# Kernel optimization log

Measured on AMD Instinct MI355X. Metric: run time of the kernel, lower is better.

Reference implementation:

```python
import jax, jax.numpy as jnp
import numpy as np
from jax import lax

INPUT, HIDDEN, OUT = 5, 32, 2

def setup_inputs() -> dict:
    key = jax.random.key(0)
    ks = jax.random.split(key, 7)
    s_ih = 1.0 / np.sqrt(HIDDEN)
    return {
        "x": jax.random.normal(ks[0], (16384, 200, INPUT), dtype=jnp.float32),
        "W_ih": jax.random.uniform(ks[1], (4 * HIDDEN, INPUT), jnp.float32, -s_ih, s_ih),
        "W_hh": jax.random.uniform(ks[2], (4 * HIDDEN, HIDDEN), jnp.float32, -s_ih, s_ih),
        "b_ih": jax.random.uniform(ks[3], (4 * HIDDEN,), jnp.float32, -s_ih, s_ih),
        "b_hh": jax.random.uniform(ks[4], (4 * HIDDEN,), jnp.float32, -s_ih, s_ih),
        "W_fc": jax.random.uniform(ks[5], (OUT, HIDDEN), jnp.float32, -s_ih, s_ih),
        "b_fc": jax.random.uniform(ks[6], (OUT,), jnp.float32, -s_ih, s_ih),
    }

def reference(x, W_ih, W_hh, b_ih, b_hh, W_fc, b_fc):
    B = x.shape[0]
    # Precompute input projections for all timesteps in one GEMM: [B,T,4H]
    x_proj = jnp.einsum("bti,gi->btg", x, W_ih) + (b_ih + b_hh)
    xs = jnp.swapaxes(x_proj, 0, 1)  # [T, B, 4H]

    def step(carry, xg):
        h, c = carry
        gates = xg + h @ W_hh.T  # [B, 4H]
        i, f, g, o = jnp.split(gates, 4, axis=-1)  # torch gate order i,f,g,o
        i = jax.nn.sigmoid(i)
        f = jax.nn.sigmoid(f)
        g = jnp.tanh(g)
        o = jax.nn.sigmoid(o)
        c = f * c + i * g
        h = o * jnp.tanh(c)
        return (h, c), None

    h0 = jnp.zeros((B, HIDDEN), x.dtype)
    c0 = jnp.zeros((B, HIDDEN), x.dtype)
    (h_n, _), _ = lax.scan(step, (h0, c0), xs)
    return h_n @ W_fc.T + b_fc  # [B, 2]
```

## Files before the change

kernel.cpp:

```cpp
#include <hip/hip_runtime.h>


typedef __bf16 bf16x8 __attribute__((ext_vector_type(8)));
typedef float  f32x4  __attribute__((ext_vector_type(4)));
typedef unsigned int u32;

constexpr int kT = 200, kIN = 5, kH = 32;
constexpr int CT   = 40;
constexpr int HSTR = 36;

union FragU {
    bf16x8 v;
    unsigned short s[8];
    u32 u[4];
};

__device__ __forceinline__ u32 bf16_rne(float f) {
    u32 u = __float_as_uint(f);
    return (u + 0x7FFFu + ((u >> 16) & 1u)) >> 16;
}
__device__ __forceinline__ float bf16f(u32 bits) { return __uint_as_float(bits << 16); }
__device__ __forceinline__ void split2(float x, u32& hi, u32& lo) {
    hi = bf16_rne(x);
    lo = bf16_rne(x - bf16f(hi));
}

__device__ __forceinline__ float sigm(float z) {
    return __builtin_amdgcn_rcpf(1.0f + __builtin_amdgcn_exp2f(-1.4426950408889634f * z));
}
__device__ __forceinline__ float tanhv(float z) {
    return fmaf(2.0f,
        __builtin_amdgcn_rcpf(1.0f + __builtin_amdgcn_exp2f(-2.8853900817779268f * z)),
        -1.0f);
}

__global__ __launch_bounds__(64, 1) void lstm_mfma(
    const float* __restrict__ x,
    const float* __restrict__ W_ih,
    const float* __restrict__ W_hh,
    const float* __restrict__ b_ih,
    const float* __restrict__ b_hh,
    const float* __restrict__ W_fc,
    const float* __restrict__ b_fc,
    float* __restrict__ out)
{
    __shared__ uint4 xbuf[CT][33];
    __shared__ u32   hbuf[16 * HSTR];

    const int lane = threadIdx.x;
    const int n16  = lane & 15;
    const int q    = lane >> 4;
    const int b0   = blockIdx.x * 16;

    bf16x8 whhh[8], whhl[8], wihf[8];
#pragma unroll
    for (int t = 0; t < 8; ++t) {
        const int r = t * 16 + n16;
        FragU H, L;
#pragma unroll
        for (int j = 0; j < 8; ++j) {
            u32 hi, lo;
            split2(W_hh[r * kH + q * 8 + j], hi, lo);
            H.s[j] = (unsigned short)hi;
            L.s[j] = (unsigned short)lo;
        }
        whhh[t] = H.v;
        whhl[t] = L.v;

        FragU F;
        F.u[0] = F.u[1] = F.u[2] = F.u[3] = 0u;
        float wr[5];
#pragma unroll
        for (int i = 0; i < 5; ++i) wr[i] = W_ih[r * kIN + i];
        u32 bh, bl;
        split2(b_ih[r] + b_hh[r], bh, bl);
        if (q == 0) {
#pragma unroll
            for (int i = 0; i < 5; ++i) F.s[i] = (unsigned short)bf16_rne(wr[i]);
#pragma unroll
            for (int i = 5; i < 8; ++i) F.s[i] = (unsigned short)bf16_rne(wr[i - 5]);
        } else if (q == 1) {
            F.s[0] = (unsigned short)bf16_rne(wr[3]);
            F.s[1] = (unsigned short)bf16_rne(wr[4]);
#pragma unroll
            for (int i = 0; i < 5; ++i) {
                u32 hi, lo; split2(wr[i], hi, lo);
                F.s[2 + i] = (unsigned short)lo;
            }
            F.s[7] = (unsigned short)bh;
        } else if (q == 2) {
            F.s[0] = (unsigned short)bl;
        }
        wihf[t] = F.v;
    }

#pragma unroll
    for (int i = 0; i < 9; ++i) hbuf[lane * 9 + i] = 0u;
    __syncthreads();

    float cst[2][4] = {{0.f, 0.f, 0.f, 0.f}, {0.f, 0.f, 0.f, 0.f}};
    const uint4* hb4 = (const uint4*)hbuf;

    for (int phase = 0; phase < kT / CT; ++phase) {
        {
            const int mm = lane >> 2, pp = lane & 3;
            const float* xrow = x + (size_t)(b0 + mm) * (kT * kIN)
                                  + (size_t)(phase * CT + pp * (CT / 4)) * kIN;
            float xv[(CT / 4) * kIN];
            const float2* xr2 = (const float2*)xrow;
#pragma unroll
            for (int i = 0; i < (CT / 4) * kIN / 2; ++i) {
                float2 v = xr2[i];
                xv[2 * i] = v.x; xv[2 * i + 1] = v.y;
            }
#pragma unroll
            for (int s5 = 0; s5 < CT / 4; ++s5) {
                u32 xh[5], xl[5];
#pragma unroll
                for (int i = 0; i < 5; ++i) split2(xv[s5 * 5 + i], xh[i], xl[i]);
                uint4 f0 = make_uint4(xh[0] | (xh[1] << 16),
                                      xh[2] | (xh[3] << 16),
                                      xh[4] | (xl[0] << 16),
                                      xl[1] | (xl[2] << 16));
                uint4 f1 = make_uint4(xl[3] | (xl[4] << 16),
                                      xh[0] | (xh[1] << 16),
                                      xh[2] | (xh[3] << 16),
                                      xh[4] | (0x3F80u << 16));
                const int tc = pp * (CT / 4) + s5;
                xbuf[tc][mm * 2 + 0] = f0;
                xbuf[tc][mm * 2 + 1] = f1;
            }
        }
        __syncthreads();

        for (int tc = 0; tc < CT; ++tc) {
            FragU xf;
            if (q < 2) {
                *(uint4*)&xf = xbuf[tc][n16 * 2 + q];
            } else if (q == 2) {
                xf.u[0] = 0x3F80u; xf.u[1] = 0u; xf.u[2] = 0u; xf.u[3] = 0u;
            } else {
                xf.u[0] = 0u; xf.u[1] = 0u; xf.u[2] = 0u; xf.u[3] = 0u;
            }

            uint4 w0 = hb4[n16 * 9 + q * 2];
            uint4 w1 = hb4[n16 * 9 + q * 2 + 1];
            FragU AH, AL;
            AH.u[0] = __builtin_amdgcn_perm(w0.y, w0.x, 0x07060302u);
            AH.u[1] = __builtin_amdgcn_perm(w0.w, w0.z, 0x07060302u);
            AH.u[2] = __builtin_amdgcn_perm(w1.y, w1.x, 0x07060302u);
            AH.u[3] = __builtin_amdgcn_perm(w1.w, w1.z, 0x07060302u);
            AL.u[0] = __builtin_amdgcn_perm(w0.y, w0.x, 0x05040100u);
            AL.u[1] = __builtin_amdgcn_perm(w0.w, w0.z, 0x05040100u);
            AL.u[2] = __builtin_amdgcn_perm(w1.y, w1.x, 0x05040100u);
            AL.u[3] = __builtin_amdgcn_perm(w1.w, w1.z, 0x05040100u);

            f32x4 acc[8];
#pragma unroll
            for (int t = 0; t < 8; ++t) {
                f32x4 a = {0.f, 0.f, 0.f, 0.f};
                a = __builtin_amdgcn_mfma_f32_16x16x32_bf16(xf.v,  wihf[t], a, 0, 0, 0);
                a = __builtin_amdgcn_mfma_f32_16x16x32_bf16(AH.v, whhh[t], a, 0, 0, 0);
                a = __builtin_amdgcn_mfma_f32_16x16x32_bf16(AH.v, whhl[t], a, 0, 0, 0);
                a = __builtin_amdgcn_mfma_f32_16x16x32_bf16(AL.v, whhh[t], a, 0, 0, 0);
                acc[t] = a;
            }

#pragma unroll
            for (int jg = 0; jg < 2; ++jg) {
#pragma unroll
                for (int r = 0; r < 4; ++r) {
                    float iv = sigm (acc[0 + jg][r]);
                    float fv = sigm (acc[2 + jg][r]);
                    float gv = tanhv(acc[4 + jg][r]);
                    float ov = sigm (acc[6 + jg][r]);
                    float cn = fmaf(fv, cst[jg][r], iv * gv);
                    cst[jg][r] = cn;
                    float hn = ov * tanhv(cn);
                    u32 hh, hl;
                    split2(hn, hh, hl);
                    hbuf[(q * 4 + r) * HSTR + n16 + 16 * jg] = (hh << 16) | hl;
                }
            }
            __syncthreads();
        }
    }

    if (lane < 32) {
        const int m = lane >> 1, o = lane & 1;
        float s = b_fc[o];
#pragma unroll
        for (int j = 0; j < kH; ++j) {
            u32 pk = hbuf[m * HSTR + j];
            float hv = bf16f(pk >> 16) + bf16f(pk & 0xFFFFu);
            s = fmaf(hv, W_fc[o * kH + j], s);
        }
        out[(size_t)(b0 + m) * 2 + o] = s;
    }
}

extern "C" void kernel_launch(void* const* d_in, const int* in_sizes, int n_in,
                              void* d_out, int out_size, void* d_ws, size_t ws_size,
                              hipStream_t stream) {
    const float* x    = (const float*)d_in[0];
    const float* W_ih = (const float*)d_in[1];
    const float* W_hh = (const float*)d_in[2];
    const float* b_ih = (const float*)d_in[3];
    const float* b_hh = (const float*)d_in[4];
    const float* W_fc = (const float*)d_in[5];
    const float* b_fc = (const float*)d_in[6];
    float* out = (float*)d_out;

    hipLaunchKernelGGL(lstm_mfma, dim3(1024), dim3(64), 0, stream,
                       x, W_ih, W_hh, b_ih, b_hh, W_fc, b_fc, out);
}
```

Before: 287.3 us.

## Split LSTM gate tiles across two waves with double-buffered split-bf16 hidden state

```diff
diff --git a/kernel.cpp b/kernel.cpp
--- a/kernel.cpp
+++ b/kernel.cpp
@@ -7,24 +7,17 @@
 
 constexpr int kT = 200, kIN = 5, kH = 32;
 constexpr int CT   = 40;
-constexpr int HSTR = 36;
-
-union FragU {
-    bf16x8 v;
-    unsigned short s[8];
-    u32 u[4];
-};
-
-__device__ __forceinline__ u32 bf16_rne(float f) {
-    u32 u = __float_as_uint(f);
-    return (u + 0x7FFFu + ((u >> 16) & 1u)) >> 16;
-}
-__device__ __forceinline__ float bf16f(u32 bits) { return __uint_as_float(bits << 16); }
-__device__ __forceinline__ void split2(float x, u32& hi, u32& lo) {
-    hi = bf16_rne(x);
-    lo = bf16_rne(x - bf16f(hi));
-}
-
+constexpr int HSTR = 40;
+
+union FragU { bf16x8 v; __bf16 b[8]; unsigned short s[8]; u32 u[4]; uint4 q4; };
+
+__device__ __forceinline__ unsigned short bfbits(__bf16 b) {
+    union { __bf16 b; unsigned short s; } u; u.b = b; return u.s;
+}
+__device__ __forceinline__ void split2(float x, __bf16& hi, __bf16& lo) {
+    hi = (__bf16)x;
+    lo = (__bf16)(x - (float)hi);
+}
 __device__ __forceinline__ float sigm(float z) {
     return __builtin_amdgcn_rcpf(1.0f + __builtin_amdgcn_exp2f(-1.4426950408889634f * z));
 }
@@ -34,7 +27,7 @@
         -1.0f);
 }
 
-__global__ __launch_bounds__(64, 1) void lstm_mfma(
+__global__ __launch_bounds__(128) void lstm_mfma2(
     const float* __restrict__ x,
     const float* __restrict__ W_ih,
     const float* __restrict__ W_hh,
@@ -45,79 +38,124 @@
     float* __restrict__ out)
 {
     __shared__ uint4 xbuf[CT][33];
-    __shared__ u32   hbuf[16 * HSTR];
-
-    const int lane = threadIdx.x;
+    __shared__ __align__(16) __bf16 hbh[2][16 * HSTR];
+    __shared__ __align__(16) __bf16 hbl[2][16 * HSTR];
+
+    const int tid  = threadIdx.x;
+    const int wv   = tid >> 6;
+    const int lane = tid & 63;
     const int n16  = lane & 15;
     const int q    = lane >> 4;
     const int b0   = blockIdx.x * 16;
 
-    bf16x8 whhh[8], whhl[8], wihf[8];
-#pragma unroll
-    for (int t = 0; t < 8; ++t) {
+    bf16x8 whhh[4], whhl[4], wihf[4];
+#pragma unroll
+    for (int g = 0; g < 4; ++g) {
+        const int t = 2 * g + wv;
         const int r = t * 16 + n16;
         FragU H, L;
 #pragma unroll
-        for (int j = 0; j < 8; ++j) {
-            u32 hi, lo;
-            split2(W_hh[r * kH + q * 8 + j], hi, lo);
-            H.s[j] = (unsigned short)hi;
-            L.s[j] = (unsigned short)lo;
-        }
-        whhh[t] = H.v;
-        whhl[t] = L.v;
+        for (int j = 0; j < 8; ++j)
+            split2(W_hh[r * kH + q * 8 + j], H.b[j], L.b[j]);
+        whhh[g] = H.v; whhl[g] = L.v;
+
+        float wr[5];
+#pragma unroll
+        for (int i = 0; i < 5; ++i) wr[i] = W_ih[r * kIN + i];
+        __bf16 bh, bl;
+        split2(b_ih[r] + b_hh[r], bh, bl);
 
         FragU F;
         F.u[0] = F.u[1] = F.u[2] = F.u[3] = 0u;
-        float wr[5];
-#pragma unroll
-        for (int i = 0; i < 5; ++i) wr[i] = W_ih[r * kIN + i];
-        u32 bh, bl;
-        split2(b_ih[r] + b_hh[r], bh, bl);
         if (q == 0) {
 #pragma unroll
-            for (int i = 0; i < 5; ++i) F.s[i] = (unsigned short)bf16_rne(wr[i]);
-#pragma unroll
-            for (int i = 5; i < 8; ++i) F.s[i] = (unsigned short)bf16_rne(wr[i - 5]);
+            for (int i = 0; i < 5; ++i) F.b[i] = (__bf16)wr[i];
+#pragma unroll
+            for (int i = 0; i < 3; ++i) F.b[5 + i] = (__bf16)wr[i];
         } else if (q == 1) {
-            F.s[0] = (unsigned short)bf16_rne(wr[3]);
-            F.s[1] = (unsigned short)bf16_rne(wr[4]);
+            F.b[0] = (__bf16)wr[3];
+            F.b[1] = (__bf16)wr[4];
 #pragma unroll
             for (int i = 0; i < 5; ++i) {
-                u32 hi, lo; split2(wr[i], hi, lo);
-                F.s[2 + i] = (unsigned short)lo;
+                __bf16 hb, lb; split2(wr[i], hb, lb);
+                F.b[2 + i] = lb;
             }
-            F.s[7] = (unsigned short)bh;
+            F.b[7] = bh;
         } else if (q == 2) {
-            F.s[0] = (unsigned short)bl;
-        }
-        wihf[t] = F.v;
-    }
-
-#pragma unroll
-    for (int i = 0; i < 9; ++i) hbuf[lane * 9 + i] = 0u;
-    __syncthreads();
-
-    float cst[2][4] = {{0.f, 0.f, 0.f, 0.f}, {0.f, 0.f, 0.f, 0.f}};
-    const uint4* hb4 = (const uint4*)hbuf;
+            F.b[0] = bl;
+        }
+        wihf[g] = F.v;
+    }
+
+    {
+        u32* z0 = (u32*)&hbh[0][0];
+        u32* z1 = (u32*)&hbl[0][0];
+        for (int i = tid; i < (16 * HSTR) / 2; i += 128) { z0[i] = 0u; z1[i] = 0u; }
+    }
+
+    float cst[4] = {0.f, 0.f, 0.f, 0.f};
+
+    const int hro = n16 * HSTR + q * 8;
+    const int hwo = (q * 4) * HSTR + n16 + 16 * wv;
+
+    auto step = [&](int tc, const __bf16* sh, const __bf16* sl,
+                    __bf16* dh, __bf16* dl) {
+        FragU xf;
+        if (q < 2) {
+            xf.q4 = xbuf[tc][n16 * 2 + q];
+        } else if (q == 2) {
+            xf.u[0] = 0x3F80u; xf.u[1] = 0u; xf.u[2] = 0u; xf.u[3] = 0u;
+        } else {
+            xf.u[0] = 0u; xf.u[1] = 0u; xf.u[2] = 0u; xf.u[3] = 0u;
+        }
+
+        bf16x8 AH = *(const bf16x8*)(sh + hro);
+        bf16x8 AL = *(const bf16x8*)(sl + hro);
+
+        f32x4 acc[4];
+#pragma unroll
+        for (int g = 0; g < 4; ++g) {
+            f32x4 a = {0.f, 0.f, 0.f, 0.f};
+            a = __builtin_amdgcn_mfma_f32_16x16x32_bf16(xf.v, wihf[g], a, 0, 0, 0);
+            a = __builtin_amdgcn_mfma_f32_16x16x32_bf16(AH,   whhh[g], a, 0, 0, 0);
+            a = __builtin_amdgcn_mfma_f32_16x16x32_bf16(AH,   whhl[g], a, 0, 0, 0);
+            a = __builtin_amdgcn_mfma_f32_16x16x32_bf16(AL,   whhh[g], a, 0, 0, 0);
+            acc[g] = a;
+        }
+
+#pragma unroll
+        for (int r = 0; r < 4; ++r) {
+            float iv = sigm (acc[0][r]);
+            float fv = sigm (acc[1][r]);
+            float gv = tanhv(acc[2][r]);
+            float ov = sigm (acc[3][r]);
+            float cn = fmaf(fv, cst[r], iv * gv);
+            cst[r] = cn;
+            float hn = ov * tanhv(cn);
+            __bf16 hh, hl;
+            split2(hn, hh, hl);
+            dh[hwo + r * HSTR] = hh;
+            dl[hwo + r * HSTR] = hl;
+        }
+        __syncthreads();
+    };
 
     for (int phase = 0; phase < kT / CT; ++phase) {
         {
-            const int mm = lane >> 2, pp = lane & 3;
+            const int mm = tid >> 3, pp = tid & 7;
             const float* xrow = x + (size_t)(b0 + mm) * (kT * kIN)
-                                  + (size_t)(phase * CT + pp * (CT / 4)) * kIN;
-            float xv[(CT / 4) * kIN];
-            const float2* xr2 = (const float2*)xrow;
-#pragma unroll
-            for (int i = 0; i < (CT / 4) * kIN / 2; ++i) {
-                float2 v = xr2[i];
-                xv[2 * i] = v.x; xv[2 * i + 1] = v.y;
-            }
-#pragma unroll
-            for (int s5 = 0; s5 < CT / 4; ++s5) {
+                                  + (size_t)(phase * CT + pp * 5) * kIN;
+            float xv[25];
+#pragma unroll
+            for (int i = 0; i < 25; ++i) xv[i] = xrow[i];
+#pragma unroll
+            for (int s5 = 0; s5 < 5; ++s5) {
                 u32 xh[5], xl[5];
 #pragma unroll
-                for (int i = 0; i < 5; ++i) split2(xv[s5 * 5 + i], xh[i], xl[i]);
+                for (int i = 0; i < 5; ++i) {
+                    __bf16 hb, lb; split2(xv[s5 * 5 + i], hb, lb);
+                    xh[i] = bfbits(hb); xl[i] = bfbits(lb);
+                }
                 uint4 f0 = make_uint4(xh[0] | (xh[1] << 16),
                                       xh[2] | (xh[3] << 16),
                                       xh[4] | (xl[0] << 16),
@@ -126,73 +164,26 @@
                                       xh[0] | (xh[1] << 16),
                                       xh[2] | (xh[3] << 16),
                                       xh[4] | (0x3F80u << 16));
-                const int tc = pp * (CT / 4) + s5;
+                const int tc = pp * 5 + s5;
                 xbuf[tc][mm * 2 + 0] = f0;
                 xbuf[tc][mm * 2 + 1] = f1;
             }
         }
         __syncthreads();
 
-        for (int tc = 0; tc < CT; ++tc) {
-            FragU xf;
-            if (q < 2) {
-                *(uint4*)&xf = xbuf[tc][n16 * 2 + q];
-            } else if (q == 2) {
-                xf.u[0] = 0x3F80u; xf.u[1] = 0u; xf.u[2] = 0u; xf.u[3] = 0u;
-            } else {
-                xf.u[0] = 0u; xf.u[1] = 0u; xf.u[2] = 0u; xf.u[3] = 0u;
-            }
-
-            uint4 w0 = hb4[n16 * 9 + q * 2];
-            uint4 w1 = hb4[n16 * 9 + q * 2 + 1];
-            FragU AH, AL;
-            AH.u[0] = __builtin_amdgcn_perm(w0.y, w0.x, 0x07060302u);
-            AH.u[1] = __builtin_amdgcn_perm(w0.w, w0.z, 0x07060302u);
-            AH.u[2] = __builtin_amdgcn_perm(w1.y, w1.x, 0x07060302u);
-            AH.u[3] = __builtin_amdgcn_perm(w1.w, w1.z, 0x07060302u);
-            AL.u[0] = __builtin_amdgcn_perm(w0.y, w0.x, 0x05040100u);
-            AL.u[1] = __builtin_amdgcn_perm(w0.w, w0.z, 0x05040100u);
-            AL.u[2] = __builtin_amdgcn_perm(w1.y, w1.x, 0x05040100u);
-            AL.u[3] = __builtin_amdgcn_perm(w1.w, w1.z, 0x05040100u);
-
-            f32x4 acc[8];
-#pragma unroll
-            for (int t = 0; t < 8; ++t) {
-                f32x4 a = {0.f, 0.f, 0.f, 0.f};
-                a = __builtin_amdgcn_mfma_f32_16x16x32_bf16(xf.v,  wihf[t], a, 0, 0, 0);
-                a = __builtin_amdgcn_mfma_f32_16x16x32_bf16(AH.v, whhh[t], a, 0, 0, 0);
-                a = __builtin_amdgcn_mfma_f32_16x16x32_bf16(AH.v, whhl[t], a, 0, 0, 0);
-                a = __builtin_amdgcn_mfma_f32_16x16x32_bf16(AL.v, whhh[t], a, 0, 0, 0);
-                acc[t] = a;
-            }
-
-#pragma unroll
-            for (int jg = 0; jg < 2; ++jg) {
-#pragma unroll
-                for (int r = 0; r < 4; ++r) {
-                    float iv = sigm (acc[0 + jg][r]);
-                    float fv = sigm (acc[2 + jg][r]);
-                    float gv = tanhv(acc[4 + jg][r]);
-                    float ov = sigm (acc[6 + jg][r]);
-                    float cn = fmaf(fv, cst[jg][r], iv * gv);
-                    cst[jg][r] = cn;
-                    float hn = ov * tanhv(cn);
-                    u32 hh, hl;
-                    split2(hn, hh, hl);
-                    hbuf[(q * 4 + r) * HSTR + n16 + 16 * jg] = (hh << 16) | hl;
-                }
-            }
-            __syncthreads();
-        }
-    }
-
-    if (lane < 32) {
-        const int m = lane >> 1, o = lane & 1;
+#pragma unroll 1
+        for (int tc = 0; tc < CT; tc += 2) {
+            step(tc,     hbh[0], hbl[0], hbh[1], hbl[1]);
+            step(tc + 1, hbh[1], hbl[1], hbh[0], hbl[0]);
+        }
+    }
+
+    if (tid < 32) {
+        const int m = tid >> 1, o = tid & 1;
         float s = b_fc[o];
 #pragma unroll
         for (int j = 0; j < kH; ++j) {
-            u32 pk = hbuf[m * HSTR + j];
-            float hv = bf16f(pk >> 16) + bf16f(pk & 0xFFFFu);
+            float hv = (float)hbh[0][m * HSTR + j] + (float)hbl[0][m * HSTR + j];
             s = fmaf(hv, W_fc[o * kH + j], s);
         }
         out[(size_t)(b0 + m) * 2 + o] = s;
@@ -211,6 +202,6 @@
     const float* b_fc = (const float*)d_in[6];
     float* out = (float*)d_out;
 
-    hipLaunchKernelGGL(lstm_mfma, dim3(1024), dim3(64), 0, stream,
+    hipLaunchKernelGGL(lstm_mfma2, dim3(1024), dim3(128), 0, stream,
                        x, W_ih, W_hh, b_ih, b_hh, W_fc, b_fc, out);
 }
```

Result: no change. 283.7 us (-1.3%).
